# Kernel optimization log

Hardware: AMD Instinct MI355X
Metric: run time of the kernel (lower is better)

## Reference

```python
import jax, jax.numpy as jnp
import numpy as np

D_MODEL = 1024
NUM_HEADS = 8
HEAD_DIM = D_MODEL // NUM_HEADS


def setup_inputs() -> dict:
    key = jax.random.key(0)
    ks = jax.random.split(key, 9)
    B, Ld, Le = 4, 1024, 2048
    s = 1.0 / np.sqrt(D_MODEL)
    return {
        "mhca_input": jax.random.normal(ks[0], (B, Ld, D_MODEL), jnp.float32),
        "encoder_output": jax.random.normal(ks[1], (B, Le, D_MODEL), jnp.float32),
        "cross_mask": jnp.zeros((B, Ld, Le), jnp.float32),
        "W_kv": jax.random.normal(ks[2], (2 * D_MODEL, D_MODEL), jnp.float32) * s,
        "b_kv": jnp.zeros((2 * D_MODEL,), jnp.float32),
        "W_q": jax.random.normal(ks[3], (D_MODEL, D_MODEL), jnp.float32) * s,
        "b_q": jnp.zeros((D_MODEL,), jnp.float32),
        "W_o": jax.random.normal(ks[4], (D_MODEL, D_MODEL), jnp.float32) * s,
        "b_o": jnp.zeros((D_MODEL,), jnp.float32),
    }


def _mhca(x, enc, mask, W_kv, b_kv, W_q, b_q, W_o, b_o):
    B, Ld, _ = x.shape
    Le = enc.shape[1]
    kv = enc @ W_kv.T + b_kv                      # [B, Le, 2*d_model]
    q = x @ W_q.T + b_q                           # [B, Ld, d_model]
    kv = kv.reshape(B, Le, NUM_HEADS, 2 * HEAD_DIM).transpose(0, 2, 1, 3)
    q = q.reshape(B, Ld, NUM_HEADS, HEAD_DIM).transpose(0, 2, 1, 3)
    k, v = kv[..., :HEAD_DIM], kv[..., HEAD_DIM:]
    scaled = jnp.einsum("bhqd,bhkd->bhqk", q, k) / np.sqrt(HEAD_DIM)
    if mask is not None:
        scaled = scaled + mask[:, None, :, :]     # == permute/add/permute in torch
    attn = jax.nn.softmax(scaled, axis=-1)
    vals = jnp.einsum("bhqk,bhkd->bhqd", attn, v)
    vals = vals.transpose(0, 2, 1, 3).reshape(B, Ld, D_MODEL)
    return vals @ W_o.T + b_o


def reference(mhca_input, encoder_output, cross_mask, W_kv, b_kv, W_q, b_q, W_o, b_o):
    return _mhca(mhca_input, encoder_output, cross_mask, W_kv, b_kv, W_q, b_q, W_o, b_o)
```

## Files before the change

kernel.cpp:

```cpp
#include <hip/hip_runtime.h>
#include <hip/hip_bf16.h>
#include <stdint.h>


#define DM   1024
#define NH   8
#define HD   128
#define LDQ  1024
#define LE   2048
#define NB   4

typedef __attribute__((ext_vector_type(8))) short bf16x8;
typedef __attribute__((ext_vector_type(4))) float f32x4;

__device__ __forceinline__ unsigned short f2bf(float f) {
  union { float f; uint32_t u; } v; v.f = f;
  uint32_t u = v.u + 0x7fffu + ((v.u >> 16) & 1u);
  return (unsigned short)(u >> 16);
}

__device__ __forceinline__ void gl_lds16(const void* g, void* l) {
  __builtin_amdgcn_global_load_lds(
      (const __attribute__((address_space(1))) void*)g,
      (__attribute__((address_space(3))) void*)l, 16, 0, 0);
}

__global__ __launch_bounds__(256) void cvt_all_kernel(
    const float* __restrict__ s0, const float* __restrict__ s1,
    const float* __restrict__ s2, const float* __restrict__ s3,
    const float* __restrict__ s4,
    unsigned short* __restrict__ d0, unsigned short* __restrict__ d1,
    unsigned short* __restrict__ d2, unsigned short* __restrict__ d3,
    unsigned short* __restrict__ d4) {
  const int total = 4194304;
  int i = blockIdx.x * blockDim.x + threadIdx.x;
  int stride = gridDim.x * blockDim.x;
  for (; i < total; i += stride) {
    const float* src; unsigned short* dst; int off;
    if (i < 1048576)      { src = s0; dst = d0; off = i; }
    else if (i < 3145728) { src = s1; dst = d1; off = i - 1048576; }
    else if (i < 3407872) { src = s2; dst = d2; off = i - 3145728; }
    else if (i < 3932160) { src = s3; dst = d3; off = i - 3407872; }
    else                  { src = s4; dst = d4; off = i - 3932160; }
    float4 v = ((const float4*)src)[off];
    ushort4 o;
    o.x = f2bf(v.x); o.y = f2bf(v.y); o.z = f2bf(v.z); o.w = f2bf(v.w);
    ((ushort4*)dst)[off] = o;
  }
}

template <int MODE>
__global__ __launch_bounds__(256) void gemm_bt(const unsigned short* __restrict__ A,
                                               const unsigned short* __restrict__ B,
                                               const float* __restrict__ bias,
                                               unsigned short* __restrict__ out0,
                                               unsigned short* __restrict__ out1,
                                               float* __restrict__ outf,
                                               int M, int N, int K) {
  __shared__ __align__(16) unsigned short As[2][128 * 32];
  __shared__ __align__(16) unsigned short Bs[2][128 * 32];
  const int tid = threadIdx.x;
  const int wave = tid >> 6, lane = tid & 63;
  const int wr = wave >> 1, wc = wave & 1;
  const int g = lane >> 4, c = lane & 15;
  const int m0 = blockIdx.y * 128, n0 = blockIdx.x * 128;

  f32x4 acc[4][4];
#pragma unroll
  for (int i = 0; i < 4; ++i)
#pragma unroll
    for (int j = 0; j < 4; ++j) acc[i][j] = (f32x4){0.f, 0.f, 0.f, 0.f};

  const unsigned short* Abase = A + (size_t)m0 * K;
  const unsigned short* Bbase = B + (size_t)n0 * K;

  auto stage = [&](int buf, int kt) {
    const unsigned short* at = Abase + kt * 32;
    const unsigned short* bt = Bbase + kt * 32;
#pragma unroll
    for (int j = 0; j < 2; ++j) {
      int chunk = wave * 2 + j;
      int o = chunk * 1024 + lane * 16;
      int os = o ^ (((o >> 6) & 3) << 4);
      int e = os >> 1;
      int row = e >> 5, col = e & 31;
      gl_lds16(at + row * K + col, (char*)(&As[buf][0]) + chunk * 1024);
      gl_lds16(bt + row * K + col, (char*)(&Bs[buf][0]) + chunk * 1024);
    }
  };

  auto compute = [&](int buf) {
    bf16x8 af[4], bfr[4];
#pragma unroll
    for (int mi = 0; mi < 4; ++mi) {
      int row = wr * 64 + mi * 16 + c;
      int byte = (row * 64 + g * 16) ^ ((row & 3) << 4);
      af[mi] = *(const bf16x8*)((const char*)&As[buf][0] + byte);
    }
#pragma unroll
    for (int ni = 0; ni < 4; ++ni) {
      int row = wc * 64 + ni * 16 + c;
      int byte = (row * 64 + g * 16) ^ ((row & 3) << 4);
      bfr[ni] = *(const bf16x8*)((const char*)&Bs[buf][0] + byte);
    }
#pragma unroll
    for (int mi = 0; mi < 4; ++mi)
#pragma unroll
      for (int ni = 0; ni < 4; ++ni)
        acc[mi][ni] = __builtin_amdgcn_mfma_f32_16x16x32_bf16(af[mi], bfr[ni],
                                                              acc[mi][ni], 0, 0, 0);
  };

  const int NT = K >> 5;
  stage(0, 0);
  __syncthreads();
  int cur = 0;
  for (int t = 0; t < NT; ++t) {
    if (t + 1 < NT) stage(cur ^ 1, t + 1);
    compute(cur);
    __syncthreads();
    cur ^= 1;
  }

#pragma unroll
  for (int mi = 0; mi < 4; ++mi) {
#pragma unroll
    for (int ni = 0; ni < 4; ++ni) {
      int n = n0 + wc * 64 + ni * 16 + c;
      float bv = bias[n];
#pragma unroll
      for (int r = 0; r < 4; ++r) {
        int m = m0 + wr * 64 + mi * 16 + g * 4 + r;
        float val = acc[mi][ni][r] + bv;
        if constexpr (MODE == 0) {
          val *= 0.08838834764831845f;
          int b = m >> 10, ld = m & 1023, h = n >> 7, d = n & 127;
          out0[((size_t)((b * 8 + h) * 1024 + ld)) * 128 + d] = f2bf(val);
        } else if constexpr (MODE == 1) {
          int b = m >> 11, le = m & 2047, h = n >> 8, w2 = n & 255;
          if (w2 < 128)
            out0[((size_t)((b * 8 + h) * 2048 + le)) * 128 + w2] = f2bf(val);
          else
            out1[((size_t)((b * 8 + h) * 128 + (w2 - 128))) * 2048 + le] = f2bf(val);
        } else {
          outf[(size_t)m * 1024 + n] = val;
        }
      }
    }
  }
}

__global__ __launch_bounds__(256) void attn_kernel(const unsigned short* __restrict__ q,
                                                   const unsigned short* __restrict__ k,
                                                   const unsigned short* __restrict__ vT,
                                                   const float* __restrict__ mask,
                                                   unsigned short* __restrict__ att) {
  __shared__ __align__(16) unsigned short Qs[64 * 128];
  __shared__ __align__(16) unsigned short Ks[64 * 128];
  __shared__ __align__(16) unsigned short Vs[128 * 64];
  __shared__ __align__(16) unsigned short Ps[4][16 * 72];

  const int tid = threadIdx.x, wave = tid >> 6, lane = tid & 63;
  const int g = lane >> 4, c = lane & 15;
  const int bh = blockIdx.y, b = bh >> 3, h = bh & 7;
  const int q0 = blockIdx.x * 64;

  const unsigned short* qbase = q + (size_t)bh * LDQ * HD + (size_t)q0 * HD;
  const unsigned short* kbase = k + (size_t)bh * LE * HD;
  const unsigned short* vbase = vT + (size_t)bh * HD * LE;
  const float* mbase = mask + ((size_t)b * LDQ + q0) * LE;

#pragma unroll
  for (int j = 0; j < 4; ++j) {
    int chunk = wave * 4 + j;
    int o = chunk * 1024 + lane * 16;
    gl_lds16(qbase + (o >> 1), (char*)Qs + chunk * 1024);
  }
  __syncthreads();

  bf16x8 qf[4];
#pragma unroll
  for (int kc = 0; kc < 4; ++kc) {
    int row = wave * 16 + c;
    qf[kc] = *(const bf16x8*)((const char*)Qs + row * 256 + kc * 64 + g * 16);
  }

  float m_run[4], l_run[4];
  f32x4 o_acc[8];
#pragma unroll
  for (int r = 0; r < 4; ++r) { m_run[r] = -1e30f; l_run[r] = 0.f; }
#pragma unroll
  for (int i = 0; i < 8; ++i) o_acc[i] = (f32x4){0.f, 0.f, 0.f, 0.f};

  for (int t = 0; t < LE / 64; ++t) {
    const int kv0 = t * 64;
#pragma unroll
    for (int j = 0; j < 4; ++j) {
      int chunk = wave * 4 + j;
      int o = chunk * 1024 + lane * 16;
      int os = o ^ (((o >> 8) & 7) << 4);
      gl_lds16(kbase + (size_t)kv0 * HD + (os >> 1), (char*)Ks + chunk * 1024);
    }
#pragma unroll
    for (int j = 0; j < 4; ++j) {
      int chunk = wave * 4 + j;
      int o = chunk * 1024 + lane * 16;
      int os = o ^ (((o >> 7) & 7) << 4);
      int e = os >> 1;
      int d = e >> 6, kvo = e & 63;
      gl_lds16(vbase + (size_t)d * LE + kv0 + kvo, (char*)Vs + chunk * 1024);
    }
    __syncthreads();

    f32x4 s[4];
#pragma unroll
    for (int n = 0; n < 4; ++n) s[n] = (f32x4){0.f, 0.f, 0.f, 0.f};
#pragma unroll
    for (int kc = 0; kc < 4; ++kc) {
#pragma unroll
      for (int n = 0; n < 4; ++n) {
        int kv = n * 16 + c;
        int byte = (kv * 256 + kc * 64 + g * 16) ^ ((kv & 7) << 4);
        bf16x8 kf = *(const bf16x8*)((const char*)Ks + byte);
        s[n] = __builtin_amdgcn_mfma_f32_16x16x32_bf16(qf[kc], kf, s[n], 0, 0, 0);
      }
    }

    float sv[4][4];
#pragma unroll
    for (int n = 0; n < 4; ++n)
#pragma unroll
      for (int r = 0; r < 4; ++r)
        sv[n][r] = s[n][r] + mbase[(size_t)(wave * 16 + g * 4 + r) * LE + kv0 + n * 16 + c];

    float pm[4];
#pragma unroll
    for (int r = 0; r < 4; ++r)
      pm[r] = fmaxf(fmaxf(sv[0][r], sv[1][r]), fmaxf(sv[2][r], sv[3][r]));
#pragma unroll
    for (int off = 1; off < 16; off <<= 1)
#pragma unroll
      for (int r = 0; r < 4; ++r) pm[r] = fmaxf(pm[r], __shfl_xor(pm[r], off));

    float mn[4], sc[4];
#pragma unroll
    for (int r = 0; r < 4; ++r) {
      mn[r] = fmaxf(m_run[r], pm[r]);
      sc[r] = __expf(m_run[r] - mn[r]);
      m_run[r] = mn[r];
    }
    float p[4][4], ps[4];
#pragma unroll
    for (int n = 0; n < 4; ++n)
#pragma unroll
      for (int r = 0; r < 4; ++r) p[n][r] = __expf(sv[n][r] - mn[r]);
#pragma unroll
    for (int r = 0; r < 4; ++r) ps[r] = p[0][r] + p[1][r] + p[2][r] + p[3][r];
#pragma unroll
    for (int off = 1; off < 16; off <<= 1)
#pragma unroll
      for (int r = 0; r < 4; ++r) ps[r] += __shfl_xor(ps[r], off);
#pragma unroll
    for (int r = 0; r < 4; ++r) l_run[r] = l_run[r] * sc[r] + ps[r];
#pragma unroll
    for (int i = 0; i < 8; ++i)
#pragma unroll
      for (int r = 0; r < 4; ++r) o_acc[i][r] *= sc[r];

#pragma unroll
    for (int n = 0; n < 4; ++n)
#pragma unroll
      for (int r = 0; r < 4; ++r)
        Ps[wave][(g * 4 + r) * 72 + n * 16 + c] = f2bf(p[n][r]);
    asm volatile("s_waitcnt lgkmcnt(0)" ::: "memory");
    __builtin_amdgcn_sched_barrier(0);

#pragma unroll
    for (int kc2 = 0; kc2 < 2; ++kc2) {
      bf16x8 pa = *(const bf16x8*)((const char*)&Ps[wave][0] + c * 144 + kc2 * 64 + g * 16);
#pragma unroll
      for (int dn = 0; dn < 8; ++dn) {
        int d = dn * 16 + c;
        int byte = (d * 128 + kc2 * 64 + g * 16) ^ ((d & 7) << 4);
        bf16x8 vf = *(const bf16x8*)((const char*)Vs + byte);
        o_acc[dn] = __builtin_amdgcn_mfma_f32_16x16x32_bf16(pa, vf, o_acc[dn], 0, 0, 0);
      }
    }
    __syncthreads();
  }

#pragma unroll
  for (int r = 0; r < 4; ++r) l_run[r] = 1.0f / l_run[r];
#pragma unroll
  for (int dn = 0; dn < 8; ++dn)
#pragma unroll
    for (int r = 0; r < 4; ++r) {
      int qrow = q0 + wave * 16 + g * 4 + r;
      att[((size_t)(b * LDQ) + qrow) * DM + h * HD + dn * 16 + c] =
          f2bf(o_acc[dn][r] * l_run[r]);
    }
}

extern "C" void kernel_launch(void* const* d_in, const int* in_sizes, int n_in,
                              void* d_out, int out_size, void* d_ws, size_t ws_size,
                              hipStream_t stream) {
  const float* x    = (const float*)d_in[0];
  const float* enc  = (const float*)d_in[1];
  const float* mask = (const float*)d_in[2];
  const float* Wkv  = (const float*)d_in[3];
  const float* bkv  = (const float*)d_in[4];
  const float* Wq   = (const float*)d_in[5];
  const float* bq   = (const float*)d_in[6];
  const float* Wo   = (const float*)d_in[7];
  const float* bo   = (const float*)d_in[8];
  float* out = (float*)d_out;

  char* ws = (char*)d_ws;
  unsigned short* x_bf   = (unsigned short*)ws; ws += (size_t)4096 * 1024 * 2;
  unsigned short* enc_bf = (unsigned short*)ws; ws += (size_t)8192 * 1024 * 2;
  unsigned short* wq_bf  = (unsigned short*)ws; ws += (size_t)1024 * 1024 * 2;
  unsigned short* wkv_bf = (unsigned short*)ws; ws += (size_t)2048 * 1024 * 2;
  unsigned short* wo_bf  = (unsigned short*)ws; ws += (size_t)1024 * 1024 * 2;
  unsigned short* q_bf   = (unsigned short*)ws; ws += (size_t)4096 * 1024 * 2;
  unsigned short* k_bf   = (unsigned short*)ws; ws += (size_t)8192 * 1024 * 2;
  unsigned short* vT_bf  = (unsigned short*)ws; ws += (size_t)8192 * 1024 * 2;
  unsigned short* att_bf = (unsigned short*)ws; ws += (size_t)4096 * 1024 * 2;

  cvt_all_kernel<<<2048, 256, 0, stream>>>(x, enc, Wq, Wkv, Wo,
                                           x_bf, enc_bf, wq_bf, wkv_bf, wo_bf);

  gemm_bt<0><<<dim3(8, 32), 256, 0, stream>>>(x_bf, wq_bf, bq, q_bf, nullptr, nullptr,
                                              4096, 1024, 1024);
  gemm_bt<1><<<dim3(16, 64), 256, 0, stream>>>(enc_bf, wkv_bf, bkv, k_bf, vT_bf, nullptr,
                                               8192, 2048, 1024);
  attn_kernel<<<dim3(16, 32), 256, 0, stream>>>(q_bf, k_bf, vT_bf, mask, att_bf);
  gemm_bt<2><<<dim3(8, 32), 256, 0, stream>>>(att_bf, wo_bf, bo, nullptr, nullptr, out,
                                              4096, 1024, 1024);
}
```

Before: 351.5 us.

## Double-buffer K/V tiles, prefetch mask, and stage mask in bf16

The attention loop now double-buffers the K and V LDS tiles and prefetches the next tile's mask values into registers, so loads overlap the MFMA compute. The mask is converted to bf16 in the conversion kernel when workspace allows, halving mask traffic in the attention kernel. Q fragments are read straight from global memory instead of through LDS. In exchange the converter does extra work, mask values are rounded to bf16, and register and LDS use go up.

```diff
diff --git a/kernel.cpp b/kernel.cpp
--- a/kernel.cpp
+++ b/kernel.cpp
@@ -18,6 +18,10 @@
   uint32_t u = v.u + 0x7fffu + ((v.u >> 16) & 1u);
   return (unsigned short)(u >> 16);
 }
+__device__ __forceinline__ float bf2f(unsigned short u) {
+  union { uint32_t u; float f; } v; v.u = ((uint32_t)u) << 16;
+  return v.f;
+}
 
 __device__ __forceinline__ void gl_lds16(const void* g, void* l) {
   __builtin_amdgcn_global_load_lds(
@@ -28,11 +32,12 @@
 __global__ __launch_bounds__(256) void cvt_all_kernel(
     const float* __restrict__ s0, const float* __restrict__ s1,
     const float* __restrict__ s2, const float* __restrict__ s3,
-    const float* __restrict__ s4,
+    const float* __restrict__ s4, const float* __restrict__ s5,
     unsigned short* __restrict__ d0, unsigned short* __restrict__ d1,
     unsigned short* __restrict__ d2, unsigned short* __restrict__ d3,
-    unsigned short* __restrict__ d4) {
-  const int total = 4194304;
+    unsigned short* __restrict__ d4, unsigned short* __restrict__ d5,
+    int do_mask) {
+  const int total = 6291456;
   int i = blockIdx.x * blockDim.x + threadIdx.x;
   int stride = gridDim.x * blockDim.x;
   for (; i < total; i += stride) {
@@ -41,7 +46,8 @@
     else if (i < 3145728) { src = s1; dst = d1; off = i - 1048576; }
     else if (i < 3407872) { src = s2; dst = d2; off = i - 3145728; }
     else if (i < 3932160) { src = s3; dst = d3; off = i - 3407872; }
-    else                  { src = s4; dst = d4; off = i - 3932160; }
+    else if (i < 4194304) { src = s4; dst = d4; off = i - 3932160; }
+    else { if (!do_mask) continue; src = s5; dst = d5; off = i - 4194304; }
     float4 v = ((const float4*)src)[off];
     ushort4 o;
     o.x = f2bf(v.x); o.y = f2bf(v.y); o.z = f2bf(v.z); o.w = f2bf(v.w);
@@ -150,14 +156,14 @@
   }
 }
 
+template <int MBF>
 __global__ __launch_bounds__(256) void attn_kernel(const unsigned short* __restrict__ q,
                                                    const unsigned short* __restrict__ k,
                                                    const unsigned short* __restrict__ vT,
-                                                   const float* __restrict__ mask,
+                                                   const void* __restrict__ maskp,
                                                    unsigned short* __restrict__ att) {
-  __shared__ __align__(16) unsigned short Qs[64 * 128];
-  __shared__ __align__(16) unsigned short Ks[64 * 128];
-  __shared__ __align__(16) unsigned short Vs[128 * 64];
+  __shared__ __align__(16) unsigned short Ks[2][64 * 128];
+  __shared__ __align__(16) unsigned short Vs[2][128 * 64];
   __shared__ __align__(16) unsigned short Ps[4][16 * 72];
 
   const int tid = threadIdx.x, wave = tid >> 6, lane = tid & 63;
@@ -168,49 +174,64 @@
   const unsigned short* qbase = q + (size_t)bh * LDQ * HD + (size_t)q0 * HD;
   const unsigned short* kbase = k + (size_t)bh * LE * HD;
   const unsigned short* vbase = vT + (size_t)bh * HD * LE;
-  const float* mbase = mask + ((size_t)b * LDQ + q0) * LE;
-
-#pragma unroll
-  for (int j = 0; j < 4; ++j) {
-    int chunk = wave * 4 + j;
-    int o = chunk * 1024 + lane * 16;
-    gl_lds16(qbase + (o >> 1), (char*)Qs + chunk * 1024);
-  }
-  __syncthreads();
+  const unsigned short* mb16 = (const unsigned short*)maskp;
+  const float* mb32 = (const float*)maskp;
+  const size_t mrowbase = ((size_t)b * LDQ + q0);
 
   bf16x8 qf[4];
-#pragma unroll
-  for (int kc = 0; kc < 4; ++kc) {
-    int row = wave * 16 + c;
-    qf[kc] = *(const bf16x8*)((const char*)Qs + row * 256 + kc * 64 + g * 16);
-  }
-
-  float m_run[4], l_run[4];
-  f32x4 o_acc[8];
-#pragma unroll
-  for (int r = 0; r < 4; ++r) { m_run[r] = -1e30f; l_run[r] = 0.f; }
-#pragma unroll
-  for (int i = 0; i < 8; ++i) o_acc[i] = (f32x4){0.f, 0.f, 0.f, 0.f};
-
-  for (int t = 0; t < LE / 64; ++t) {
-    const int kv0 = t * 64;
+  {
+    const int qrow = wave * 16 + c;
+#pragma unroll
+    for (int kc = 0; kc < 4; ++kc)
+      qf[kc] = *(const bf16x8*)(qbase + (size_t)qrow * HD + kc * 32 + g * 8);
+  }
+
+  auto stage_kv = [&](int buf, int t) {
 #pragma unroll
     for (int j = 0; j < 4; ++j) {
       int chunk = wave * 4 + j;
       int o = chunk * 1024 + lane * 16;
-      int os = o ^ (((o >> 8) & 7) << 4);
-      gl_lds16(kbase + (size_t)kv0 * HD + (os >> 1), (char*)Ks + chunk * 1024);
-    }
-#pragma unroll
-    for (int j = 0; j < 4; ++j) {
-      int chunk = wave * 4 + j;
-      int o = chunk * 1024 + lane * 16;
-      int os = o ^ (((o >> 7) & 7) << 4);
-      int e = os >> 1;
+      int osk = o ^ (((o >> 8) & 7) << 4);
+      gl_lds16(kbase + (size_t)t * 64 * HD + (osk >> 1),
+               (char*)&Ks[buf][0] + chunk * 1024);
+      int osv = o ^ (((o >> 7) & 7) << 4);
+      int e = osv >> 1;
       int d = e >> 6, kvo = e & 63;
-      gl_lds16(vbase + (size_t)d * LE + kv0 + kvo, (char*)Vs + chunk * 1024);
-    }
-    __syncthreads();
+      gl_lds16(vbase + (size_t)d * LE + t * 64 + kvo,
+               (char*)&Vs[buf][0] + chunk * 1024);
+    }
+  };
+
+  float mcur[16], mnext[16];
+  auto load_mask = [&](int t, float* mr) {
+#pragma unroll
+    for (int n = 0; n < 4; ++n)
+#pragma unroll
+      for (int r = 0; r < 4; ++r) {
+        size_t idx = (mrowbase + wave * 16 + g * 4 + r) * LE + t * 64 + n * 16 + c;
+        if constexpr (MBF) mr[n * 4 + r] = bf2f(mb16[idx]);
+        else               mr[n * 4 + r] = mb32[idx];
+      }
+  };
+
+  float m_run[4], l_run[4];
+  f32x4 o_acc[8];
+#pragma unroll
+  for (int r = 0; r < 4; ++r) { m_run[r] = -1e30f; l_run[r] = 0.f; }
+#pragma unroll
+  for (int i = 0; i < 8; ++i) o_acc[i] = (f32x4){0.f, 0.f, 0.f, 0.f};
+
+  stage_kv(0, 0);
+  load_mask(0, mcur);
+  __syncthreads();
+
+  int cur = 0;
+  const int NT = LE / 64;
+  for (int t = 0; t < NT; ++t) {
+    if (t + 1 < NT) {
+      stage_kv(cur ^ 1, t + 1);
+      load_mask(t + 1, mnext);
+    }
 
     f32x4 s[4];
 #pragma unroll
@@ -221,7 +242,7 @@
       for (int n = 0; n < 4; ++n) {
         int kv = n * 16 + c;
         int byte = (kv * 256 + kc * 64 + g * 16) ^ ((kv & 7) << 4);
-        bf16x8 kf = *(const bf16x8*)((const char*)Ks + byte);
+        bf16x8 kf = *(const bf16x8*)((const char*)&Ks[cur][0] + byte);
         s[n] = __builtin_amdgcn_mfma_f32_16x16x32_bf16(qf[kc], kf, s[n], 0, 0, 0);
       }
     }
@@ -230,8 +251,7 @@
 #pragma unroll
     for (int n = 0; n < 4; ++n)
 #pragma unroll
-      for (int r = 0; r < 4; ++r)
-        sv[n][r] = s[n][r] + mbase[(size_t)(wave * 16 + g * 4 + r) * LE + kv0 + n * 16 + c];
+      for (int r = 0; r < 4; ++r) sv[n][r] = s[n][r] + mcur[n * 4 + r];
 
     float pm[4];
 #pragma unroll
@@ -282,11 +302,15 @@
       for (int dn = 0; dn < 8; ++dn) {
         int d = dn * 16 + c;
         int byte = (d * 128 + kc2 * 64 + g * 16) ^ ((d & 7) << 4);
-        bf16x8 vf = *(const bf16x8*)((const char*)Vs + byte);
+        bf16x8 vf = *(const bf16x8*)((const char*)&Vs[cur][0] + byte);
         o_acc[dn] = __builtin_amdgcn_mfma_f32_16x16x32_bf16(pa, vf, o_acc[dn], 0, 0, 0);
       }
     }
+
     __syncthreads();
+    cur ^= 1;
+#pragma unroll
+    for (int i = 0; i < 16; ++i) mcur[i] = mnext[i];
   }
 
 #pragma unroll
@@ -316,24 +340,32 @@
   float* out = (float*)d_out;
 
   char* ws = (char*)d_ws;
-  unsigned short* x_bf   = (unsigned short*)ws; ws += (size_t)4096 * 1024 * 2;
-  unsigned short* enc_bf = (unsigned short*)ws; ws += (size_t)8192 * 1024 * 2;
-  unsigned short* wq_bf  = (unsigned short*)ws; ws += (size_t)1024 * 1024 * 2;
-  unsigned short* wkv_bf = (unsigned short*)ws; ws += (size_t)2048 * 1024 * 2;
-  unsigned short* wo_bf  = (unsigned short*)ws; ws += (size_t)1024 * 1024 * 2;
-  unsigned short* q_bf   = (unsigned short*)ws; ws += (size_t)4096 * 1024 * 2;
-  unsigned short* k_bf   = (unsigned short*)ws; ws += (size_t)8192 * 1024 * 2;
-  unsigned short* vT_bf  = (unsigned short*)ws; ws += (size_t)8192 * 1024 * 2;
-  unsigned short* att_bf = (unsigned short*)ws; ws += (size_t)4096 * 1024 * 2;
-
-  cvt_all_kernel<<<2048, 256, 0, stream>>>(x, enc, Wq, Wkv, Wo,
-                                           x_bf, enc_bf, wq_bf, wkv_bf, wo_bf);
+  unsigned short* x_bf    = (unsigned short*)ws; ws += (size_t)4096 * 1024 * 2;
+  unsigned short* enc_bf  = (unsigned short*)ws; ws += (size_t)8192 * 1024 * 2;
+  unsigned short* wq_bf   = (unsigned short*)ws; ws += (size_t)1024 * 1024 * 2;
+  unsigned short* wkv_bf  = (unsigned short*)ws; ws += (size_t)2048 * 1024 * 2;
+  unsigned short* wo_bf   = (unsigned short*)ws; ws += (size_t)1024 * 1024 * 2;
+  unsigned short* q_bf    = (unsigned short*)ws; ws += (size_t)4096 * 1024 * 2;
+  unsigned short* k_bf    = (unsigned short*)ws; ws += (size_t)8192 * 1024 * 2;
+  unsigned short* vT_bf   = (unsigned short*)ws; ws += (size_t)8192 * 1024 * 2;
+  unsigned short* att_bf  = (unsigned short*)ws; ws += (size_t)4096 * 1024 * 2;
+  unsigned short* mask_bf = (unsigned short*)ws; ws += (size_t)8192 * 1024 * 2;
+
+  const size_t need = (size_t)(ws - (char*)d_ws);
+  const int use_bf_mask = (ws_size >= need) ? 1 : 0;
+
+  cvt_all_kernel<<<2048, 256, 0, stream>>>(x, enc, Wq, Wkv, Wo, mask,
+                                           x_bf, enc_bf, wq_bf, wkv_bf, wo_bf,
+                                           mask_bf, use_bf_mask);
 
   gemm_bt<0><<<dim3(8, 32), 256, 0, stream>>>(x_bf, wq_bf, bq, q_bf, nullptr, nullptr,
                                               4096, 1024, 1024);
   gemm_bt<1><<<dim3(16, 64), 256, 0, stream>>>(enc_bf, wkv_bf, bkv, k_bf, vT_bf, nullptr,
                                                8192, 2048, 1024);
-  attn_kernel<<<dim3(16, 32), 256, 0, stream>>>(q_bf, k_bf, vT_bf, mask, att_bf);
+  if (use_bf_mask)
+    attn_kernel<1><<<dim3(16, 32), 256, 0, stream>>>(q_bf, k_bf, vT_bf, mask_bf, att_bf);
+  else
+    attn_kernel<0><<<dim3(16, 32), 256, 0, stream>>>(q_bf, k_bf, vT_bf, mask, att_bf);
   gemm_bt<2><<<dim3(8, 32), 256, 0, stream>>>(att_bf, wo_bf, bo, nullptr, nullptr, out,
                                               4096, 1024, 1024);
 }
```

Result: slower. 359.2 us (+2.2%).
